# Performance work log

Hardware: AMD Instinct MI355X
Metric: run time of the kernel (lower is better)

## Reference

```python
import jax, jax.numpy as jnp
import numpy as np

PI = np.pi
F0 = 0.91  # Fresnel base reflectance (Schlick), NeRFactor default
EH, EW = 16, 32  # env map lat/long resolution


def normalize(x, eps=1e-8):
    return x / (jnp.linalg.norm(x, axis=-1, keepdims=True) + eps)


def safe_div(num, den):
    # divide_no_nan semantics, grad-safe
    ok = jnp.abs(den) > 1e-12
    return jnp.where(ok, num / jnp.where(ok, den, 1.0), 0.0)


def sample_envmap(probe, dirs):
    # Equirectangular bilinear sample. probe: [eH,eW,3]; dirs: [...,3] normalized.
    eH, eW = probe.shape[0], probe.shape[1]
    z = jnp.clip(dirs[..., 2], -1.0 + 1e-6, 1.0 - 1e-6)
    theta = jnp.arccos(z)                       # [0, pi]
    phi = jnp.arctan2(dirs[..., 1], dirs[..., 0])  # (-pi, pi]
    v = theta / PI * eH - 0.5
    u = (phi / (2.0 * PI) + 0.5) * eW - 0.5
    v0 = jnp.floor(v); u0 = jnp.floor(u)
    fv = (v - v0)[..., None]; fu = (u - u0)[..., None]
    v0i = jnp.clip(v0.astype(jnp.int32), 0, eH - 1)
    v1i = jnp.clip(v0i + 1, 0, eH - 1)
    u0i = jnp.mod(u0.astype(jnp.int32), eW)
    u1i = jnp.mod(u0i + 1, eW)
    p00 = probe[v0i, u0i]; p01 = probe[v0i, u1i]
    p10 = probe[v1i, u0i]; p11 = probe[v1i, u1i]
    return (p00 * (1 - fu) + p01 * fu) * (1 - fv) + (p10 * (1 - fu) + p11 * fu) * fv


def microfacet_brdf(pts2l, pts2c, normal, albedo, rough):
    # pts2l: [B,eH,eW,P,3]; pts2c, normal: [B,P,3]; albedo: [B,P,3]; rough: [B,P,1]
    c = pts2c[:, None, None]   # [B,1,1,P,3]
    n = normal[:, None, None]  # [B,1,1,P,3]
    h = normalize(pts2l + c)   # half vector [B,eH,eW,P,3]
    # Fresnel (Schlick)
    l_dot_h = jnp.sum(pts2l * h, -1)
    f = F0 + (1.0 - F0) * (1.0 - l_dot_h) ** 5
    alpha = (rough ** 2)[..., 0][:, None, None]  # [B,1,1,P]
    # D (GGX normal distribution)
    cos_m = jnp.sum(h * n, -1)
    chi_m = (cos_m > 0).astype(h.dtype)
    cos_m_sq = cos_m ** 2
    tan_m_sq = safe_div(1.0 - cos_m_sq, cos_m_sq)
    d = safe_div(alpha ** 2 * chi_m, PI * cos_m_sq ** 2 * (alpha ** 2 + tan_m_sq) ** 2)
    # G (GGX geometric term, NeRFactor style)
    cos_v = jnp.sum(normal * pts2c, -1)[:, None, None]  # [B,1,1,P]
    cos_hv = jnp.sum(h * c, -1)
    chi_g = (safe_div(cos_hv, cos_v) > 0).astype(h.dtype)
    cos_v_sq = jnp.clip(cos_v ** 2, 0.0, 1.0)
    tan_v_sq = jnp.clip(safe_div(1.0 - cos_v_sq, cos_v_sq), 0.0, 1e10)
    g = safe_div(chi_g * 2.0, 1.0 + jnp.sqrt(1.0 + alpha ** 2 * tan_v_sq))
    l_dot_n = jnp.sum(pts2l * n, -1)
    micro = safe_div(f * g * d, 4.0 * jnp.abs(l_dot_n) * jnp.abs(cos_v))
    # glossy + lambertian diffuse
    return micro[..., None] + (albedo / PI)[:, None, None]  # [B,eH,eW,P,3]


def linear2srgb(x):
    x = jnp.clip(x, 0.0, 1.0)
    return jnp.where(x <= 0.0031308, 12.92 * x,
                     1.055 * jnp.power(jnp.maximum(x, 1e-8), 1.0 / 2.4) - 0.055)


def setup_inputs() -> dict:
    key = jax.random.key(0)
    ks = jax.random.split(key, 12)
    B, P, Pt = 1, 8192, 65536
    surf = jax.random.normal(ks[0], (B, P, 3), jnp.float32)
    ray_o = jax.random.normal(ks[1], (B, P, 3), jnp.float32) + 3.0
    norm_raw = jax.random.normal(ks[2], (B, P, 3), jnp.float32)
    albedo = jax.random.uniform(ks[3], (B, P, 3), jnp.float32)
    roughness = 0.1 + 0.9 * jax.random.uniform(ks[4], (B, P, 1), jnp.float32)
    lvis = jax.random.uniform(ks[5], (B, P, EH * EW), jnp.float32)
    xyz = jax.random.normal(ks[6], (EH, EW, 3), jnp.float32) * 10.0
    area = jax.random.uniform(ks[7], (EH, EW), jnp.float32)
    probe = jax.random.uniform(ks[8], (EH, EW, 3), jnp.float32)
    grd_rgb = jax.random.uniform(ks[9], (B, Pt, 3), jnp.float32)
    grd_acc = jax.random.uniform(ks[10], (B, Pt), jnp.float32)
    inds = jnp.sort(jax.random.randint(ks[11], (B, P), 0, Pt, jnp.int32), axis=-1)
    return {"surf": surf, "ray_o": ray_o, "norm_raw": norm_raw, "albedo": albedo,
            "roughness": roughness, "lvis": lvis, "xyz": xyz, "area": area,
            "probe": probe, "grd_rgb": grd_rgb, "grd_acc": grd_acc, "inds": inds}


def reference(surf, ray_o, norm_raw, albedo, roughness, lvis, xyz, area, probe,
              grd_rgb, grd_acc, inds):
    B, P, _ = surf.shape
    eH, eW, _ = xyz.shape
    norm = normalize(norm_raw)
    # lvis: [B,P,L] -> [B,eH,eW,P]
    lvis_g = jnp.transpose(lvis, (0, 2, 1)).reshape(B, eH, eW, P)
    ldir = normalize(xyz)[None, :, :, None]             # [1,eH,eW,1,3]
    ldot = jnp.sum(ldir * norm[:, None, None], -1)      # [B,eH,eW,P]
    surf2light = normalize(xyz[:, :, None] - surf[:, None, None])  # [B,eH,eW,P,3]
    surf2cam = normalize(ray_o - surf)                  # [B,P,3]
    light = sample_envmap(probe, surf2light)            # [B,eH,eW,P,3]
    shade = lvis_g[..., None] * ldot[..., None] * area[None, :, :, None, None] * light
    brdf = microfacet_brdf(surf2light, surf2cam, norm, albedo, roughness)
    rgb = jnp.sum(brdf * shade, axis=(1, 2))            # [B,P,3]
    rgb = linear2srgb(rgb)
    # alpha_blend: scatter shaded rays into ground image, blend by ground acc
    bidx = jnp.arange(B)[:, None]
    scatter = jnp.zeros_like(grd_rgb).at[bidx, inds].set(rgb)
    acc = grd_acc[..., None]
    merged = grd_rgb * acc + scatter * (1.0 - acc)      # [B,Pt,3]
    return merged
```

## Files before the change

### kernel.cpp

```cpp
#include <hip/hip_runtime.h>
#include <math.h>

#define NL     512
#define EH_C   16
#define EW_C   32
#define P_PTS  8192
#define PT_PTS 65536
#define PROW   33
#define PTILE  (17*33)
#define RBLK   1024

typedef float f32x2 __attribute__((ext_vector_type(2)));

__device__ __forceinline__ float rcp_f(float x)  { return __builtin_amdgcn_rcpf(x); }
__device__ __forceinline__ float rsq_f(float x)  { return __builtin_amdgcn_rsqf(x); }
__device__ __forceinline__ float sqrt_f(float x) { return __builtin_amdgcn_sqrtf(x); }

__device__ __forceinline__ f32x2 rcp2(f32x2 x)  { return (f32x2){rcp_f(x.x),  rcp_f(x.y)}; }
__device__ __forceinline__ f32x2 rsq2(f32x2 x)  { return (f32x2){rsq_f(x.x),  rsq_f(x.y)}; }
__device__ __forceinline__ f32x2 sqrt2(f32x2 x) { return (f32x2){sqrt_f(x.x), sqrt_f(x.y)}; }
__device__ __forceinline__ f32x2 floor2(f32x2 x){ return (f32x2){floorf(x.x), floorf(x.y)}; }
__device__ __forceinline__ f32x2 abs2(f32x2 x)  { return (f32x2){fabsf(x.x),  fabsf(x.y)}; }
__device__ __forceinline__ f32x2 max2(f32x2 a, f32x2 b){ return (f32x2){fmaxf(a.x,b.x), fmaxf(a.y,b.y)}; }
__device__ __forceinline__ f32x2 min2(f32x2 a, f32x2 b){ return (f32x2){fminf(a.x,b.x), fminf(a.y,b.y)}; }
__device__ __forceinline__ f32x2 maxs(f32x2 a, float b){ return (f32x2){fmaxf(a.x,b), fmaxf(a.y,b)}; }

__global__ __launch_bounds__(256, 4) void fused_kernel(
    const float* __restrict__ surf,
    const float* __restrict__ ray_o,
    const float* __restrict__ norm_raw,
    const float* __restrict__ albedo,
    const float* __restrict__ rough,
    const float* __restrict__ lvis,
    const float* __restrict__ xyz,
    const float* __restrict__ area,
    const float* __restrict__ probe,
    const float* __restrict__ grd_rgb,
    const float* __restrict__ grd_acc,
    const int*   __restrict__ inds,
    float* __restrict__ out)
{
    if (blockIdx.x >= RBLK) {
        int row = (blockIdx.x - RBLK) * 256 + threadIdx.x;
        int lo = 0, hi = P_PTS;
        while (lo < hi) { int mid = (lo + hi) >> 1; if (inds[mid] < row) lo = mid + 1; else hi = mid; }
        bool scattered = (lo < P_PTS) && (inds[lo] == row);
        if (!scattered) {
            float a = grd_acc[row];
            out[3*row+0] = grd_rgb[3*row+0] * a;
            out[3*row+1] = grd_rgb[3*row+1] * a;
            out[3*row+2] = grd_rgb[3*row+2] * a;
        }
        return;
    }

    __shared__ float4 sA[NL];
    __shared__ float4 sP2[PTILE];

    for (int i = threadIdx.x; i < NL; i += 256) {
        float x = xyz[3*i+0], y = xyz[3*i+1], z = xyz[3*i+2];
        float aw = area[i] / (sqrtf(x*x + y*y + z*z) + 1e-8f);
        sA[i] = make_float4(x, y, z, aw);
    }
    for (int i = threadIdx.x; i < PTILE; i += 256) {
        int vr = i / PROW;
        int ur = i - vr * PROW;
        int sv = vr > 15 ? 15 : vr;
        int su = ur & 31;
        int t  = 3 * (sv * EW_C + su);
        sP2[i] = make_float4(probe[t], probe[t+1], probe[t+2], 0.0f);
    }
    __syncthreads();

    const int lane  = threadIdx.x & 63;
    const int pbase = blockIdx.x * 8 + ((threadIdx.x >> 6) << 1);

    #pragma clang loop unroll(disable)
    for (int sub = 0; sub < 2; ++sub) {
        const int p = pbase + sub;

        float sx = surf[3*p+0], sy = surf[3*p+1], sz = surf[3*p+2];
        float nx = norm_raw[3*p+0], ny = norm_raw[3*p+1], nz = norm_raw[3*p+2];
        { float inv = 1.0f / (sqrtf(nx*nx + ny*ny + nz*nz) + 1e-8f); nx*=inv; ny*=inv; nz*=inv; }
        float cx = ray_o[3*p+0]-sx, cy = ray_o[3*p+1]-sy, cz = ray_o[3*p+2]-sz;
        { float inv = 1.0f / (sqrtf(cx*cx + cy*cy + cz*cz) + 1e-8f); cx*=inv; cy*=inv; cz*=inv; }

        float cos_v  = nx*cx + ny*cy + nz*cz;
        float r      = rough[p];
        float alpha2 = (r*r)*(r*r);
        float cvsq   = fminf(fmaxf(cos_v*cos_v, 0.0f), 1.0f);
        float tvsq   = (cvsq > 1e-12f) ? fminf((1.0f - cvsq)/cvsq, 1e10f) : 0.0f;
        float gden   = 1.0f + sqrtf(1.0f + alpha2 * tvsq);
        float g2a    = (cos_v > 1e-12f) ? (2.0f / gden) * alpha2 * 0.3183098862f : 0.0f;
        float a2m1   = alpha2 - 1.0f;
        float acv4   = 4.0f * fabsf(cos_v);
        float ab0 = albedo[3*p+0] * 0.3183098862f;
        float ab1 = albedo[3*p+1] * 0.3183098862f;
        float ab2 = albedo[3*p+2] * 0.3183098862f;
        const float* lv = lvis + p*NL;

        f32x2 acc0 = (f32x2)(0.0f), acc1 = (f32x2)(0.0f), acc2 = (f32x2)(0.0f);

        #pragma unroll
        for (int it = 0; it < 4; ++it) {
            int l0 = it*128 + (lane << 1);
            float2 lvv = *reinterpret_cast<const float2*>(lv + l0);
            float4 A0 = sA[l0], A1 = sA[l0+1];
            f32x2 Ax = {A0.x, A1.x}, Ay = {A0.y, A1.y}, Az = {A0.z, A1.z}, Aw = {A0.w, A1.w};

            f32x2 dx = Ax - sx, dy = Ay - sy, dz = Az - sz;
            f32x2 inv = rsq2(dx*dx + dy*dy + dz*dz);
            f32x2 slx = dx*inv, sly = dy*inv, slz = dz*inv;

            f32x2 sh = ((f32x2){lvv.x, lvv.y}) * (Ax*nx + Ay*ny + Az*nz) * Aw;

            f32x2 zc = min2(maxs(slz, -0.999999f), (f32x2)(0.999999f));
            f32x2 xa = abs2(zc);
            f32x2 pcl = xa*-0.00642982f + 0.03397049f;
            pcl = pcl*xa - 0.08702911f;
            pcl = pcl*xa + 0.15733105f;
            pcl = pcl*xa - 0.25553564f;
            pcl = pcl*xa + 0.45316427f;
            pcl = pcl*xa - 1.09294280f;
            pcl = pcl*xa + 7.99999960f;
            f32x2 vpre = sqrt2(1.0f - xa) * pcl;
            f32x2 vv;
            vv.x = (zc.x < 0.0f) ? (15.5f - vpre.x) : (vpre.x - 0.5f);
            vv.y = (zc.y < 0.0f) ? (15.5f - vpre.y) : (vpre.y - 0.5f);

            f32x2 axv = abs2(slx), ayv = abs2(sly);
            f32x2 mx = max2(axv, ayv), mn = min2(axv, ayv);
            f32x2 a  = mn * rcp2(maxs(mx, 1e-37f));
            f32x2 s  = a * a;
            f32x2 pu = s*-0.0596956f + 0.2681612f;
            pu = pu*s - 0.5929877f;
            pu = pu*s + 0.9857085f;
            pu = pu*s - 1.6940397f;
            pu = pu*s + 5.0928424f;
            f32x2 rk = a * pu;
            rk.x = (ayv.x > axv.x) ? 8.0f  - rk.x : rk.x;
            rk.y = (ayv.y > axv.y) ? 8.0f  - rk.y : rk.y;
            rk.x = (slx.x < 0.0f)  ? 16.0f - rk.x : rk.x;
            rk.y = (slx.y < 0.0f)  ? 16.0f - rk.y : rk.y;
            f32x2 uu = { copysignf(rk.x, sly.x) + 15.5f,
                         copysignf(rk.y, sly.y) + 15.5f };

            f32x2 v0f = floor2(vv), u0f = floor2(uu);
            f32x2 fv = vv - v0f, fu = uu - u0f;
            f32x2 w11 = fu*fv, w10 = fv - w11, w01 = fu - w11;
            f32x2 w00 = (1.0f - fu) - w10;

            f32x2 hdot = slx*cx + sly*cy + slz*cz;
            f32x2 ih   = rsq2(maxs(hdot*2.0f + 2.0f, 1e-12f));
            f32x2 ldh  = (1.0f + hdot) * ih;
            f32x2 ldn  = slx*nx + sly*ny + slz*nz;
            f32x2 cm   = (ldn + cos_v) * ih;
            f32x2 om   = 1.0f - ldh;
            f32x2 om2  = om*om;
            f32x2 ff   = om2*om2*om*0.09f + 0.91f;
            f32x2 q    = cm*cm*a2m1 + 1.0f;
            f32x2 den  = abs2(ldn) * acv4;
            f32x2 micro = ff * g2a * rcp2(q*q*den);
            micro.x = (cm.x > 1e-6f && den.x > 1e-12f) ? micro.x : 0.0f;
            micro.y = (cm.y > 1e-6f && den.y > 1e-12f) ? micro.y : 0.0f;

            int v0a = (int)v0f.x; v0a = v0a < 0 ? 0 : v0a;
            int u0a = ((int)u0f.x) & 31;
            int v0b = (int)v0f.y; v0b = v0b < 0 ? 0 : v0b;
            int u0b = ((int)u0f.y) & 31;
            const float4* pa = &sP2[v0a*PROW + u0a];
            const float4* pb = &sP2[v0b*PROW + u0b];
            float4 t00a = pa[0], t01a = pa[1], t10a = pa[PROW], t11a = pa[PROW+1];
            float4 t00b = pb[0], t01b = pb[1], t10b = pb[PROW], t11b = pb[PROW+1];

            f32x2 li0 = { fmaf(t00a.x,w00.x, fmaf(t01a.x,w01.x, fmaf(t10a.x,w10.x, t11a.x*w11.x))),
                          fmaf(t00b.x,w00.y, fmaf(t01b.x,w01.y, fmaf(t10b.x,w10.y, t11b.x*w11.y))) };
            f32x2 li1 = { fmaf(t00a.y,w00.x, fmaf(t01a.y,w01.x, fmaf(t10a.y,w10.x, t11a.y*w11.x))),
                          fmaf(t00b.y,w00.y, fmaf(t01b.y,w01.y, fmaf(t10b.y,w10.y, t11b.y*w11.y))) };
            f32x2 li2 = { fmaf(t00a.z,w00.x, fmaf(t01a.z,w01.x, fmaf(t10a.z,w10.x, t11a.z*w11.x))),
                          fmaf(t00b.z,w00.y, fmaf(t01b.z,w01.y, fmaf(t10b.z,w10.y, t11b.z*w11.y))) };

            acc0 += (micro + ab0) * (sh * li0);
            acc1 += (micro + ab1) * (sh * li1);
            acc2 += (micro + ab2) * (sh * li2);
        }

        float c0 = acc0.x + acc0.y;
        float c1 = acc1.x + acc1.y;
        float c2 = acc2.x + acc2.y;

        for (int off = 32; off > 0; off >>= 1) {
            c0 += __shfl_xor(c0, off);
            c1 += __shfl_xor(c1, off);
            c2 += __shfl_xor(c2, off);
        }

        if (lane == 0) {
            int idx = inds[p];
            bool last = (p == P_PTS-1) || (inds[p+1] != idx);
            if (last) {
                float a = grd_acc[idx];
                float rgb[3] = {c0, c1, c2};
                #pragma unroll
                for (int c = 0; c < 3; ++c) {
                    float x = fminf(fmaxf(rgb[c], 0.0f), 1.0f);
                    float sr = (x <= 0.0031308f)
                             ? 12.92f * x
                             : fmaf(1.055f, exp2f(log2f(x) * (1.0f/2.4f)), -0.055f);
                    out[3*idx+c] = fmaf(grd_rgb[3*idx+c], a, sr * (1.0f - a));
                }
            }
        }
    }
}

extern "C" void kernel_launch(void* const* d_in, const int* in_sizes, int n_in,
                              void* d_out, int out_size, void* d_ws, size_t ws_size,
                              hipStream_t stream) {
    const float* surf      = (const float*)d_in[0];
    const float* ray_o     = (const float*)d_in[1];
    const float* norm_raw  = (const float*)d_in[2];
    const float* albedo    = (const float*)d_in[3];
    const float* roughness = (const float*)d_in[4];
    const float* lvis      = (const float*)d_in[5];
    const float* xyz       = (const float*)d_in[6];
    const float* area      = (const float*)d_in[7];
    const float* probe     = (const float*)d_in[8];
    const float* grd_rgb   = (const float*)d_in[9];
    const float* grd_acc   = (const float*)d_in[10];
    const int*   inds      = (const int*)d_in[11];
    float* out = (float*)d_out;

    fused_kernel<<<RBLK + PT_PTS/256, 256, 0, stream>>>(surf, ray_o, norm_raw,
        albedo, roughness, lvis, xyz, area, probe, grd_rgb, grd_acc, inds, out);
}
```

Baseline: 22.78 us.

## Pack env-map bilinear quads as fp16 and fold ground-fill work into shading blocks

The env-map cache in shared memory is rebuilt as one record per cell holding all four bilinear neighbours, packed as fp16 (RG in a uint4, B in a uint2). Each sample then needs two wide LDS reads instead of four float4 reads, and shared memory per block shrinks. The separate ground-only blocks are removed, and each shading block's first wavefront now does the binary-search fill for 64 output rows at its end. This trades probe precision (fp16 rounding of radiance) for less LDS traffic, and appends a tail of serial work to every shading block.

```diff
diff --git a/kernel.cpp b/kernel.cpp
--- a/kernel.cpp
+++ b/kernel.cpp
@@ -1,4 +1,5 @@
 #include <hip/hip_runtime.h>
+#include <hip/hip_fp16.h>
 #include <math.h>
 
 #define NL     512
@@ -6,8 +7,6 @@
 #define EW_C   32
 #define P_PTS  8192
 #define PT_PTS 65536
-#define PROW   33
-#define PTILE  (17*33)
 #define RBLK   1024
 
 typedef float f32x2 __attribute__((ext_vector_type(2)));
@@ -24,6 +23,10 @@
 __device__ __forceinline__ f32x2 max2(f32x2 a, f32x2 b){ return (f32x2){fmaxf(a.x,b.x), fmaxf(a.y,b.y)}; }
 __device__ __forceinline__ f32x2 min2(f32x2 a, f32x2 b){ return (f32x2){fminf(a.x,b.x), fminf(a.y,b.y)}; }
 __device__ __forceinline__ f32x2 maxs(f32x2 a, float b){ return (f32x2){fmaxf(a.x,b), fmaxf(a.y,b)}; }
+
+__device__ __forceinline__ float2 h2f(unsigned int u) {
+    return __half22float2(*reinterpret_cast<const __half2*>(&u));
+}
 
 __global__ __launch_bounds__(256, 4) void fused_kernel(
     const float* __restrict__ surf,
@@ -40,35 +43,36 @@
     const int*   __restrict__ inds,
     float* __restrict__ out)
 {
-    if (blockIdx.x >= RBLK) {
-        int row = (blockIdx.x - RBLK) * 256 + threadIdx.x;
-        int lo = 0, hi = P_PTS;
-        while (lo < hi) { int mid = (lo + hi) >> 1; if (inds[mid] < row) lo = mid + 1; else hi = mid; }
-        bool scattered = (lo < P_PTS) && (inds[lo] == row);
-        if (!scattered) {
-            float a = grd_acc[row];
-            out[3*row+0] = grd_rgb[3*row+0] * a;
-            out[3*row+1] = grd_rgb[3*row+1] * a;
-            out[3*row+2] = grd_rgb[3*row+2] * a;
-        }
-        return;
-    }
-
     __shared__ float4 sA[NL];
-    __shared__ float4 sP2[PTILE];
+    __shared__ uint4  sQrg[NL];
+    __shared__ uint2  sQb [NL];
 
     for (int i = threadIdx.x; i < NL; i += 256) {
         float x = xyz[3*i+0], y = xyz[3*i+1], z = xyz[3*i+2];
         float aw = area[i] / (sqrtf(x*x + y*y + z*z) + 1e-8f);
         sA[i] = make_float4(x, y, z, aw);
-    }
-    for (int i = threadIdx.x; i < PTILE; i += 256) {
-        int vr = i / PROW;
-        int ur = i - vr * PROW;
-        int sv = vr > 15 ? 15 : vr;
-        int su = ur & 31;
-        int t  = 3 * (sv * EW_C + su);
-        sP2[i] = make_float4(probe[t], probe[t+1], probe[t+2], 0.0f);
+
+        int v  = i >> 5, u = i & 31;
+        int v1 = v + 1 > 15 ? 15 : v + 1;
+        int u1 = (u + 1) & 31;
+        int t00 = 3*((v <<5) + u),  t01 = 3*((v <<5) + u1);
+        int t10 = 3*((v1<<5) + u),  t11 = 3*((v1<<5) + u1);
+        __half2 h00 = __floats2half2_rn(probe[t00], probe[t00+1]);
+        __half2 h01 = __floats2half2_rn(probe[t01], probe[t01+1]);
+        __half2 h10 = __floats2half2_rn(probe[t10], probe[t10+1]);
+        __half2 h11 = __floats2half2_rn(probe[t11], probe[t11+1]);
+        uint4 q;
+        q.x = *reinterpret_cast<unsigned int*>(&h00);
+        q.y = *reinterpret_cast<unsigned int*>(&h01);
+        q.z = *reinterpret_cast<unsigned int*>(&h10);
+        q.w = *reinterpret_cast<unsigned int*>(&h11);
+        sQrg[i] = q;
+        __half2 b01 = __floats2half2_rn(probe[t00+2], probe[t01+2]);
+        __half2 b23 = __floats2half2_rn(probe[t10+2], probe[t11+2]);
+        uint2 qb;
+        qb.x = *reinterpret_cast<unsigned int*>(&b01);
+        qb.y = *reinterpret_cast<unsigned int*>(&b23);
+        sQb[i] = qb;
     }
     __syncthreads();
 
@@ -168,17 +172,22 @@
             int u0a = ((int)u0f.x) & 31;
             int v0b = (int)v0f.y; v0b = v0b < 0 ? 0 : v0b;
             int u0b = ((int)u0f.y) & 31;
-            const float4* pa = &sP2[v0a*PROW + u0a];
-            const float4* pb = &sP2[v0b*PROW + u0b];
-            float4 t00a = pa[0], t01a = pa[1], t10a = pa[PROW], t11a = pa[PROW+1];
-            float4 t00b = pb[0], t01b = pb[1], t10b = pb[PROW], t11b = pb[PROW+1];
-
-            f32x2 li0 = { fmaf(t00a.x,w00.x, fmaf(t01a.x,w01.x, fmaf(t10a.x,w10.x, t11a.x*w11.x))),
-                          fmaf(t00b.x,w00.y, fmaf(t01b.x,w01.y, fmaf(t10b.x,w10.y, t11b.x*w11.y))) };
-            f32x2 li1 = { fmaf(t00a.y,w00.x, fmaf(t01a.y,w01.x, fmaf(t10a.y,w10.x, t11a.y*w11.x))),
-                          fmaf(t00b.y,w00.y, fmaf(t01b.y,w01.y, fmaf(t10b.y,w10.y, t11b.y*w11.y))) };
-            f32x2 li2 = { fmaf(t00a.z,w00.x, fmaf(t01a.z,w01.x, fmaf(t10a.z,w10.x, t11a.z*w11.x))),
-                          fmaf(t00b.z,w00.y, fmaf(t01b.z,w01.y, fmaf(t10b.z,w10.y, t11b.z*w11.y))) };
+            int cella = (v0a << 5) + u0a;
+            int cellb = (v0b << 5) + u0b;
+            uint4 qa = sQrg[cella], qb = sQrg[cellb];
+            uint2 ba = sQb[cella],  bb = sQb[cellb];
+
+            float2 rg00a = h2f(qa.x), rg01a = h2f(qa.y), rg10a = h2f(qa.z), rg11a = h2f(qa.w);
+            float2 rg00b = h2f(qb.x), rg01b = h2f(qb.y), rg10b = h2f(qb.z), rg11b = h2f(qb.w);
+            float2 b01a  = h2f(ba.x), b23a  = h2f(ba.y);
+            float2 b01b  = h2f(bb.x), b23b  = h2f(bb.y);
+
+            f32x2 li0 = { fmaf(rg00a.x,w00.x, fmaf(rg01a.x,w01.x, fmaf(rg10a.x,w10.x, rg11a.x*w11.x))),
+                          fmaf(rg00b.x,w00.y, fmaf(rg01b.x,w01.y, fmaf(rg10b.x,w10.y, rg11b.x*w11.y))) };
+            f32x2 li1 = { fmaf(rg00a.y,w00.x, fmaf(rg01a.y,w01.x, fmaf(rg10a.y,w10.x, rg11a.y*w11.x))),
+                          fmaf(rg00b.y,w00.y, fmaf(rg01b.y,w01.y, fmaf(rg10b.y,w10.y, rg11b.y*w11.y))) };
+            f32x2 li2 = { fmaf(b01a.x,w00.x, fmaf(b01a.y,w01.x, fmaf(b23a.x,w10.x, b23a.y*w11.x))),
+                          fmaf(b01b.x,w00.y, fmaf(b01b.y,w01.y, fmaf(b23b.x,w10.y, b23b.y*w11.y))) };
 
             acc0 += (micro + ab0) * (sh * li0);
             acc1 += (micro + ab1) * (sh * li1);
@@ -210,6 +219,19 @@
                     out[3*idx+c] = fmaf(grd_rgb[3*idx+c], a, sr * (1.0f - a));
                 }
             }
+        }
+    }
+
+    if (threadIdx.x < 64) {
+        int row = blockIdx.x * 64 + threadIdx.x;
+        int lo = 0, hi = P_PTS;
+        while (lo < hi) { int mid = (lo + hi) >> 1; if (inds[mid] < row) lo = mid + 1; else hi = mid; }
+        bool scattered = (lo < P_PTS) && (inds[lo] == row);
+        if (!scattered) {
+            float a = grd_acc[row];
+            out[3*row+0] = grd_rgb[3*row+0] * a;
+            out[3*row+1] = grd_rgb[3*row+1] * a;
+            out[3*row+2] = grd_rgb[3*row+2] * a;
         }
     }
 }
@@ -231,6 +253,6 @@
     const int*   inds      = (const int*)d_in[11];
     float* out = (float*)d_out;
 
-    fused_kernel<<<RBLK + PT_PTS/256, 256, 0, stream>>>(surf, ray_o, norm_raw,
+    fused_kernel<<<RBLK, 256, 0, stream>>>(surf, ray_o, norm_raw,
         albedo, roughness, lvis, xyz, area, probe, grd_rgb, grd_acc, inds, out);
 }
```

Measured after the change: 24.06 us. 5.6% more time.
